# Kernel optimization log

Measured on AMD Instinct MI355X. Metric: run time of the kernel, lower is better.

Reference implementation:

```python
import jax, jax.numpy as jnp
import numpy as np

BITS = 256      # bits per token
HEADS = 8       # num voting heads
NPOS = 4        # n_position_bits for RELATIVE encoder (binary code of distance)
MAXD = 8        # max_distance of position encoder
NBPN = 12       # n_bits_per_neuron = min(similarity_bits, 12)
SEQ = 2048      # number of tokens
SIM = 2 * BITS + NPOS  # similarity_bits


def setup_inputs() -> dict:
    key = jax.random.key(0)
    k1, k2, k3 = jax.random.split(key, 3)
    tokens = jax.random.randint(k1, (SEQ, BITS), 0, 2, dtype=jnp.int32)
    head_idx = jax.random.randint(k2, (HEADS, NBPN), 0, SIM, dtype=jnp.int32)
    # RAM table contents: one bit (0/1) per address per head (trained lookup table)
    table = jax.random.bernoulli(k3, 0.5, (HEADS, 2 ** NBPN)).astype(jnp.float32)
    return {"tokens": tokens, "head_idx": head_idx, "table": table}


def reference(tokens, head_idx, table):
    S, B = tokens.shape
    H, K = head_idx.shape
    w = (2 ** jnp.arange(K)).astype(jnp.int32)  # slot weight 2^k per selected bit

    # relative-distance binary code table for distances 0..MAXD  -> (MAXD+1, NPOS)
    d_vals = jnp.arange(MAXD + 1)
    rel_bits = ((d_vals[:, None] >> jnp.arange(NPOS)[None, :]) & 1).astype(jnp.int32)

    # which source each selected bit position comes from within cat([query,key,rel])
    mask_q = (head_idx < B)
    mask_k = (head_idx >= B) & (head_idx < 2 * B)
    mask_r = head_idx >= 2 * B

    qg = tokens[:, jnp.clip(head_idx, 0, B - 1)]            # (S, H, K)
    kg = tokens[:, jnp.clip(head_idx - B, 0, B - 1)]        # (S, H, K)
    rg = rel_bits[:, jnp.clip(head_idx - 2 * B, 0, NPOS - 1)]  # (MAXD+1, H, K)

    # separable address contributions (query / key / relative distance)
    Aq = jnp.einsum('shk,hk->sh', qg, (mask_q * w).astype(jnp.int32))  # (S, H)
    Ak = jnp.einsum('shk,hk->sh', kg, (mask_k * w).astype(jnp.int32))  # (S, H)
    Ar = jnp.einsum('dhk,hk->dh', rg, (mask_r * w).astype(jnp.int32))  # (MAXD+1, H)

    i = jnp.arange(S)
    dist = jnp.clip(i[:, None] - i[None, :], 0, MAXD)        # (S, S)
    addr = Aq[:, None, :] + Ak[None, :, :] + Ar[dist]        # (S, S, H)

    head_votes = table[jnp.arange(H)[None, None, :], addr]   # (S, S, H)
    tril = (i[None, :] <= i[:, None]).astype(table.dtype)    # j > i gets vote 0
    votes = head_votes.sum(-1) * tril                        # (S, S)

    thr = H // 2
    attended = (votes >= thr).astype(table.dtype)            # (S, S)
    included = attended.sum(-1)                              # (S,)

    tok_f = tokens.astype(table.dtype)
    # XOR of selected tokens == per-bit parity of their sum
    parity = jnp.mod(attended @ tok_f, 2.0)                  # (S, B)
    # fallback: first token with max vote when nothing crossed the threshold
    fallback = tok_f[jnp.argmax(votes, axis=-1)]             # (S, B)
    return jnp.where((included > 0)[:, None], parity, fallback)
```

## Files before the change

### kernel.cpp

```cpp
#include <hip/hip_runtime.h>
#include <stdint.h>

#define SEQ   2048
#define BITS  256
#define HEADS 8
#define NPOS  4
#define MAXD  8
#define NBPN  12

typedef unsigned long long u64;
typedef unsigned int       u32;
typedef unsigned short     u16;

#define OFF_TBL    0
#define OFF_PACKED 4096
#define OFF_AQ     (4096 + 65536)
#define OFF_AK     (4096 + 65536 + 32768)
#define OFF_AR     (4096 + 65536 + 65536)

__global__ __launch_bounds__(256) void prep_kernel(
        const int* __restrict__ tokens, const int* __restrict__ head_idx,
        const float* __restrict__ table,
        u64* __restrict__ tblbits, u64* __restrict__ packed,
        u16* __restrict__ Aq, u16* __restrict__ Ak, u16* __restrict__ Ar) {
    const int bid = blockIdx.x, tid = threadIdx.x;
    if (bid < 2048) {
        int t = bid * 256 + tid;
        u64 m = __ballot(tokens[t] & 1);
        if ((tid & 63) == 0) packed[t >> 6] = m;
    } else if (bid < 2048 + 128) {
        int t = (bid - 2048) * 256 + tid;
        u64 m = __ballot(table[t] != 0.0f);
        if ((tid & 63) == 0) tblbits[t >> 6] = m;
    } else {
        int t = (bid - 2176) * 256 + tid;
        int s = t >> 3, h = t & 7;
        const int* hi  = head_idx + h * NBPN;
        const int* tok = tokens + s * BITS;
        int aq = 0, ak = 0;
        #pragma unroll
        for (int k = 0; k < NBPN; ++k) {
            int idx = hi[k];
            if (idx < BITS)          aq += tok[idx] << k;
            else if (idx < 2 * BITS) ak += tok[idx - BITS] << k;
        }
        Aq[t] = (u16)aq;
        Ak[t] = (u16)ak;
        if (t < (MAXD + 1) * HEADS) {
            int d = t / HEADS, hh = t % HEADS;
            const int* hi2 = head_idx + hh * NBPN;
            int ar = 0;
            #pragma unroll
            for (int k = 0; k < NBPN; ++k) {
                int idx = hi2[k];
                if (idx >= 2 * BITS) ar += ((d >> (idx - 2 * BITS)) & 1) << k;
            }
            Ar[t] = (u16)ar;
        }
    }
}

__device__ inline u64 shfl_down_u64(u64 x, int o) {
    u32 lo = (u32)x, hi = (u32)(x >> 32);
    lo = __shfl_down(lo, o, 64);
    hi = __shfl_down(hi, o, 64);
    return ((u64)hi << 32) | lo;
}

__global__ __launch_bounds__(128) void row_kernel(
        const u64* __restrict__ tblbits, const u64* __restrict__ packed,
        const u16* __restrict__ Aq, const u16* __restrict__ Ak,
        const u16* __restrict__ Ar, float* __restrict__ out) {

    __shared__ u32 tbl[HEADS * 128];
    __shared__ u16 aqar[MAXD + 1][HEADS];
    __shared__ u64 p_acc[2][4];
    __shared__ int p_inc[2];
    __shared__ u64 p_key[2];

    const int i   = blockIdx.x;
    const int tid = threadIdx.x;

    const u32* tb32 = (const u32*)tblbits;
    #pragma unroll
    for (int w = 0; w < 8; ++w) tbl[tid + w * 128] = tb32[tid + w * 128];
    if (tid < (MAXD + 1) * HEADS) {
        int h = tid & 7;
        aqar[tid >> 3][h] = (u16)(Aq[i * HEADS + h] + Ar[tid]);
    }
    __syncthreads();

    u32 a8[8];
    #pragma unroll
    for (int h = 0; h < 8; ++h) a8[h] = aqar[MAXD][h];

    u64 acc0 = 0, acc1 = 0, acc2 = 0, acc3 = 0;
    int inc = 0;
    u64 bestkey = 0;

    if (tid < MAXD) {
        int j = i - tid;
        if (j >= 0) {
            const uint4 akv = *(const uint4*)(Ak + j * HEADS);
            int votes = 0;
            #pragma unroll
            for (int h = 0; h < 8; ++h) {
                u32 ak_h = ((&akv.x)[h >> 1] >> ((h & 1) * 16)) & 0xFFFFu;
                u32 addr = (u32)aqar[tid][h] + ak_h;
                votes += (int)((tbl[(h << 7) + (addr >> 5)] >> (addr & 31)) & 1u);
            }
            int att = (votes >= HEADS / 2) ? 1 : 0;
            u64 m = (u64)0 - (u64)att;
            const ulonglong2* pj = (const ulonglong2*)(packed + j * 4);
            ulonglong2 pA = pj[0], pB = pj[1];
            acc0 ^= pA.x & m; acc1 ^= pA.y & m;
            acc2 ^= pB.x & m; acc3 ^= pB.y & m;
            inc += att;
            u64 key = ((u64)(votes + 1) << 32) | (u64)(0x7FFFFFFF - j);
            if (key > bestkey) bestkey = key;
        }
    }

    const int ilim = i - MAXD;
    int j = tid;
    uint4 akv; ulonglong2 pA, pB;
    if (j <= ilim) {
        akv = *(const uint4*)(Ak + j * HEADS);
        const ulonglong2* pj = (const ulonglong2*)(packed + j * 4);
        pA = pj[0]; pB = pj[1];
    }
    while (j <= ilim) {
        const int jn = j + 128;
        uint4 akv_n; ulonglong2 pA_n, pB_n;
        if (jn <= ilim) {
            akv_n = *(const uint4*)(Ak + jn * HEADS);
            const ulonglong2* pjn = (const ulonglong2*)(packed + jn * 4);
            pA_n = pjn[0]; pB_n = pjn[1];
        }
        int votes = 0;
        #pragma unroll
        for (int h = 0; h < 8; ++h) {
            u32 ak_h = ((&akv.x)[h >> 1] >> ((h & 1) * 16)) & 0xFFFFu;
            u32 addr = a8[h] + ak_h;
            votes += (int)((tbl[(h << 7) + (addr >> 5)] >> (addr & 31)) & 1u);
        }
        int att = (votes >= HEADS / 2) ? 1 : 0;
        u64 m = (u64)0 - (u64)att;
        acc0 ^= pA.x & m; acc1 ^= pA.y & m;
        acc2 ^= pB.x & m; acc3 ^= pB.y & m;
        inc += att;
        u64 key = ((u64)(votes + 1) << 32) | (u64)(0x7FFFFFFF - j);
        if (key > bestkey) bestkey = key;
        j = jn; akv = akv_n; pA = pA_n; pB = pB_n;
    }

    #pragma unroll
    for (int o = 32; o > 0; o >>= 1) {
        acc0 ^= shfl_down_u64(acc0, o);
        acc1 ^= shfl_down_u64(acc1, o);
        acc2 ^= shfl_down_u64(acc2, o);
        acc3 ^= shfl_down_u64(acc3, o);
        inc  += __shfl_down(inc, o, 64);
        u64 k2 = shfl_down_u64(bestkey, o);
        if (k2 > bestkey) bestkey = k2;
    }
    int wave = tid >> 6;
    if ((tid & 63) == 0) {
        p_acc[wave][0] = acc0; p_acc[wave][1] = acc1;
        p_acc[wave][2] = acc2; p_acc[wave][3] = acc3;
        p_inc[wave] = inc; p_key[wave] = bestkey;
    }
    __syncthreads();

    u64 f0 = p_acc[0][0] ^ p_acc[1][0];
    u64 f1 = p_acc[0][1] ^ p_acc[1][1];
    u64 f2 = p_acc[0][2] ^ p_acc[1][2];
    u64 f3 = p_acc[0][3] ^ p_acc[1][3];
    int finc = p_inc[0] + p_inc[1];
    u64 fk = (p_key[0] > p_key[1]) ? p_key[0] : p_key[1];

    int b0   = tid * 2;
    int wsel = tid >> 5;
    u64 word;
    if (finc > 0) {
        word = (wsel < 2) ? (wsel == 0 ? f0 : f1) : (wsel == 2 ? f2 : f3);
    } else {
        int bestj = 0x7FFFFFFF - (int)(fk & 0xFFFFFFFFu);
        word = packed[bestj * 4 + wsel];
    }
    int sh = b0 & 63;
    float2 o2 = make_float2((float)((word >> sh) & 1ull),
                            (float)((word >> (sh + 1)) & 1ull));
    *(float2*)(out + i * BITS + b0) = o2;
}

extern "C" void kernel_launch(void* const* d_in, const int* in_sizes, int n_in,
                              void* d_out, int out_size, void* d_ws, size_t ws_size,
                              hipStream_t stream) {
    const int*   tokens   = (const int*)d_in[0];
    const int*   head_idx = (const int*)d_in[1];
    const float* table    = (const float*)d_in[2];
    float*       out      = (float*)d_out;
    char*        ws       = (char*)d_ws;

    u64* tblbits = (u64*)(ws + OFF_TBL);
    u64* packed  = (u64*)(ws + OFF_PACKED);
    u16* Aq      = (u16*)(ws + OFF_AQ);
    u16* Ak      = (u16*)(ws + OFF_AK);
    u16* Ar      = (u16*)(ws + OFF_AR);

    prep_kernel<<<2240, 256, 0, stream>>>(tokens, head_idx, table,
                                          tblbits, packed, Aq, Ak, Ar);
    row_kernel <<<SEQ, 128, 0, stream>>>(tblbits, packed, Aq, Ak, Ar, out);
}
```

Measured before the change: 75.70 us.

## Assign one query row per wavefront and reduce with xor shuffles

New measurement: 78.79 us. 4.1% more time.

```diff
diff --git a/kernel.cpp b/kernel.cpp
--- a/kernel.cpp
+++ b/kernel.cpp
@@ -60,10 +60,10 @@
     }
 }
 
-__device__ inline u64 shfl_down_u64(u64 x, int o) {
+__device__ inline u64 shfl_xor_u64(u64 x, int o) {
     u32 lo = (u32)x, hi = (u32)(x >> 32);
-    lo = __shfl_down(lo, o, 64);
-    hi = __shfl_down(hi, o, 64);
+    lo = __shfl_xor(lo, o, 64);
+    hi = __shfl_xor(hi, o, 64);
     return ((u64)hi << 32) | lo;
 }
 
@@ -73,40 +73,38 @@
         const u16* __restrict__ Ar, float* __restrict__ out) {
 
     __shared__ u32 tbl[HEADS * 128];
-    __shared__ u16 aqar[MAXD + 1][HEADS];
-    __shared__ u64 p_acc[2][4];
-    __shared__ int p_inc[2];
-    __shared__ u64 p_key[2];
-
-    const int i   = blockIdx.x;
-    const int tid = threadIdx.x;
+    __shared__ u16 aqar[2][MAXD + 1][HEADS];
+
+    const int tid  = threadIdx.x;
+    const int lane = tid & 63, w = tid >> 6;
+    const int i    = blockIdx.x * 2 + w;
 
     const u32* tb32 = (const u32*)tblbits;
     #pragma unroll
-    for (int w = 0; w < 8; ++w) tbl[tid + w * 128] = tb32[tid + w * 128];
-    if (tid < (MAXD + 1) * HEADS) {
-        int h = tid & 7;
-        aqar[tid >> 3][h] = (u16)(Aq[i * HEADS + h] + Ar[tid]);
+    for (int q = 0; q < 8; ++q) tbl[tid + q * 128] = tb32[tid + q * 128];
+    for (int e = lane; e < (MAXD + 1) * HEADS; e += 64) {
+        int h = e & 7;
+        aqar[w][e >> 3][h] = (u16)(Aq[i * HEADS + h] + Ar[e]);
     }
     __syncthreads();
 
     u32 a8[8];
     #pragma unroll
-    for (int h = 0; h < 8; ++h) a8[h] = aqar[MAXD][h];
+    for (int h = 0; h < 8; ++h) a8[h] = aqar[w][MAXD][h];
 
     u64 acc0 = 0, acc1 = 0, acc2 = 0, acc3 = 0;
     int inc = 0;
     u64 bestkey = 0;
 
-    if (tid < MAXD) {
-        int j = i - tid;
+    if (lane < MAXD) {
+        int j = i - lane;
         if (j >= 0) {
             const uint4 akv = *(const uint4*)(Ak + j * HEADS);
             int votes = 0;
             #pragma unroll
             for (int h = 0; h < 8; ++h) {
                 u32 ak_h = ((&akv.x)[h >> 1] >> ((h & 1) * 16)) & 0xFFFFu;
-                u32 addr = (u32)aqar[tid][h] + ak_h;
+                u32 addr = (u32)aqar[w][lane][h] + ak_h;
                 votes += (int)((tbl[(h << 7) + (addr >> 5)] >> (addr & 31)) & 1u);
             }
             int att = (votes >= HEADS / 2) ? 1 : 0;
@@ -122,7 +120,7 @@
     }
 
     const int ilim = i - MAXD;
-    int j = tid;
+    int j = lane;
     uint4 akv; ulonglong2 pA, pB;
     if (j <= ilim) {
         akv = *(const uint4*)(Ak + j * HEADS);
@@ -130,7 +128,7 @@
         pA = pj[0]; pB = pj[1];
     }
     while (j <= ilim) {
-        const int jn = j + 128;
+        const int jn = j + 64;
         uint4 akv_n; ulonglong2 pA_n, pB_n;
         if (jn <= ilim) {
             akv_n = *(const uint4*)(Ak + jn * HEADS);
@@ -155,43 +153,31 @@
     }
 
     #pragma unroll
-    for (int o = 32; o > 0; o >>= 1) {
-        acc0 ^= shfl_down_u64(acc0, o);
-        acc1 ^= shfl_down_u64(acc1, o);
-        acc2 ^= shfl_down_u64(acc2, o);
-        acc3 ^= shfl_down_u64(acc3, o);
-        inc  += __shfl_down(inc, o, 64);
-        u64 k2 = shfl_down_u64(bestkey, o);
+    for (int o = 1; o < 64; o <<= 1) {
+        acc0 ^= shfl_xor_u64(acc0, o);
+        acc1 ^= shfl_xor_u64(acc1, o);
+        acc2 ^= shfl_xor_u64(acc2, o);
+        acc3 ^= shfl_xor_u64(acc3, o);
+        inc  += __shfl_xor(inc, o, 64);
+        u64 k2 = shfl_xor_u64(bestkey, o);
         if (k2 > bestkey) bestkey = k2;
     }
-    int wave = tid >> 6;
-    if ((tid & 63) == 0) {
-        p_acc[wave][0] = acc0; p_acc[wave][1] = acc1;
-        p_acc[wave][2] = acc2; p_acc[wave][3] = acc3;
-        p_inc[wave] = inc; p_key[wave] = bestkey;
-    }
-    __syncthreads();
-
-    u64 f0 = p_acc[0][0] ^ p_acc[1][0];
-    u64 f1 = p_acc[0][1] ^ p_acc[1][1];
-    u64 f2 = p_acc[0][2] ^ p_acc[1][2];
-    u64 f3 = p_acc[0][3] ^ p_acc[1][3];
-    int finc = p_inc[0] + p_inc[1];
-    u64 fk = (p_key[0] > p_key[1]) ? p_key[0] : p_key[1];
-
-    int b0   = tid * 2;
-    int wsel = tid >> 5;
+
+    int wsel = lane >> 4;
     u64 word;
-    if (finc > 0) {
-        word = (wsel < 2) ? (wsel == 0 ? f0 : f1) : (wsel == 2 ? f2 : f3);
+    if (inc > 0) {
+        word = (wsel < 2) ? (wsel == 0 ? acc0 : acc1)
+                          : (wsel == 2 ? acc2 : acc3);
     } else {
-        int bestj = 0x7FFFFFFF - (int)(fk & 0xFFFFFFFFu);
+        int bestj = 0x7FFFFFFF - (int)(bestkey & 0xFFFFFFFFu);
         word = packed[bestj * 4 + wsel];
     }
-    int sh = b0 & 63;
-    float2 o2 = make_float2((float)((word >> sh) & 1ull),
-                            (float)((word >> (sh + 1)) & 1ull));
-    *(float2*)(out + i * BITS + b0) = o2;
+    int sh = (lane & 15) * 4;
+    float4 o4 = make_float4((float)((word >> sh) & 1ull),
+                            (float)((word >> (sh + 1)) & 1ull),
+                            (float)((word >> (sh + 2)) & 1ull),
+                            (float)((word >> (sh + 3)) & 1ull));
+    *(float4*)(out + i * BITS + lane * 4) = o4;
 }
 
 extern "C" void kernel_launch(void* const* d_in, const int* in_sizes, int n_in,
@@ -211,5 +197,5 @@
 
     prep_kernel<<<2240, 256, 0, stream>>>(tokens, head_idx, table,
                                           tblbits, packed, Aq, Ak, Ar);
-    row_kernel <<<SEQ, 128, 0, stream>>>(tblbits, packed, Aq, Ak, Ar, out);
-}
+    row_kernel <<<SEQ / 2, 128, 0, stream>>>(tblbits, packed, Aq, Ak, Ar, out);
+}
```
